# Kernel tuning notes

Hardware: AMD Instinct MI355X
Metric: run time of the kernel (lower is better)

Reference implementation:

```python
import jax, jax.numpy as jnp
import numpy as np

EPS_LOG = 1e-10
DECAY = 0.99
RESET_THRESHOLD = 2


def setup_inputs() -> dict:
    key = jax.random.key(0)
    ks = jax.random.split(key, 8)
    B, C_in, T = 4, 1024, 2048
    K, D = 8192, 256
    N = B * T
    return {
        "z": jax.random.normal(ks[0], (B, C_in, T), dtype=jnp.float32),
        "u": jax.random.uniform(ks[1], (N, K), dtype=jnp.float32),
        "Wi": jax.random.normal(ks[2], (D, C_in), dtype=jnp.float32) * 0.02,
        "bi": jax.random.normal(ks[3], (D,), dtype=jnp.float32) * 0.02,
        "Wo": jax.random.normal(ks[4], (C_in, D), dtype=jnp.float32) * 0.02,
        "bo": jax.random.normal(ks[5], (C_in,), dtype=jnp.float32) * 0.02,
        "embedding": jax.random.normal(ks[6], (K, D), dtype=jnp.float32),
        "cluster_size": jnp.zeros((K,), dtype=jnp.float32),
    }


def reference(z, u, Wi, bi, Wo, bo, embedding, cluster_size):
    B, _, T = z.shape
    K, D = embedding.shape
    N = B * T

    # inproj: Conv1d with kernel_size=1 == pointwise linear over channel dim
    z_e = jnp.einsum('bit,di->bdt', z, Wi) + bi[None, :, None]  # (B, D, T)
    z_d = z_e.transpose(0, 2, 1).reshape(N, D)                   # (b t) d

    # squared-euclidean distances via norm expansion
    dist = ((z_d ** 2).sum(axis=1, keepdims=True)
            - 2.0 * (z_d @ embedding.T)
            + (embedding ** 2).sum(axis=1))                      # (N, K)

    # gumbel noise (training=True), softmax_temp = 1.0
    gumbel = -jnp.log(-jnp.log(u + EPS_LOG) + EPS_LOG)
    logits = -dist + gumbel
    y_soft = jax.nn.softmax(logits, axis=-1)                     # (N, K)

    z_q_flat = y_soft @ embedding                                # (N, D)

    # kl_div(log(avg+eps), uniform target of shape (N,K), reduction='sum')
    avg_probs = y_soft.mean(axis=0)                              # (K,)
    inv_k = 1.0 / K
    kl_loss = N * jnp.sum(inv_k * (jnp.log(inv_k) - jnp.log(avg_probs + EPS_LOG)))

    indices = jnp.argmax(y_soft, axis=1)                         # (N,) int

    z_q = z_q_flat.reshape(B, T, D).transpose(0, 2, 1)           # (B, D, T)
    vq_loss = jnp.mean((z_e - jax.lax.stop_gradient(z_q)) ** 2)

    # outproj: Conv1d kernel_size=1
    out = jnp.einsum('bdt,od->bot', z_q, Wo) + bo[None, :, None]  # (B, C_in, T)

    # box_result: active_num uses cluster_size BEFORE the EMA update
    active_num = (cluster_size > RESET_THRESHOLD).sum().astype(z.dtype)
    counts = jnp.zeros((K,), z.dtype).at[indices].add(1.0)       # one-hot column sums
    probs = counts / N                                           # == mean(one_hot, axis=0)
    perplexity = jnp.exp(-jnp.sum(probs * jnp.log(probs + EPS_LOG)))
    new_cluster_size = cluster_size * DECAY + counts * (1.0 - DECAY)

    return out, vq_loss, kl_loss, perplexity, active_num, new_cluster_size
```

## Files before the change

kernel.cpp:

```cpp
#include <hip/hip_runtime.h>
#include <hip/hip_fp16.h>


#define NROWS 8192
#define KCL   8192
#define DDIM  256
#define CIN   1024
#define TSEQ  2048
#define EPSL  1e-10f
#define MHAT  (-140.0f)

#define OUT_SC   (4*CIN*TSEQ)

#define ZD_OFF   0
#define ZQ_OFF   (NROWS*DDIM)
#define E2_OFF   (2*NROWS*DDIM)
#define CS_OFF   (E2_OFF + KCL)
#define CNT_OFF  (CS_OFF + KCL)
#define VQ_OFF   (CNT_OFF + KCL)
#define LINV_OFF (VQ_OFF + 4)

#define ZD2W   0
#define ZQ2W   2097152
#define EBW    4194304
#define ETW    5242880
#define WOBW   6291456
#define ZFW    6422528
#define E2W    7471104
#define C2W    7479296
#define LINVW  7487488
#define CSUMW  7495680
#define CNTW   7503872
#define VQW    7512064
#define PW     7512128
#define ENDW   (PW + 33554432)

using short8v = __attribute__((ext_vector_type(8))) short;
using short4v = __attribute__((ext_vector_type(4))) short;
using f32x16  = __attribute__((ext_vector_type(16))) float;

__device__ __forceinline__ ushort f2bf(float f) {
  unsigned int x = __float_as_uint(f);
  return (ushort)((x + 0x7FFFu + ((x >> 16) & 1u)) >> 16);
}
__device__ __forceinline__ float bf2f(ushort h) {
  return __uint_as_float(((unsigned int)h) << 16);
}
__device__ __forceinline__ short8v pack8(float4 a, float4 b) {
  short8v v;
  v[0] = (short)f2bf(a.x); v[1] = (short)f2bf(a.y);
  v[2] = (short)f2bf(a.z); v[3] = (short)f2bf(a.w);
  v[4] = (short)f2bf(b.x); v[5] = (short)f2bf(b.y);
  v[6] = (short)f2bf(b.z); v[7] = (short)f2bf(b.w);
  return v;
}
__device__ __forceinline__ void gload16(const void* g, void* l) {
  __builtin_amdgcn_global_load_lds(
      (const __attribute__((address_space(1))) unsigned int*)g,
      (__attribute__((address_space(3))) unsigned int*)l, 16, 0, 0);
}


__global__ __launch_bounds__(256) void e2_kernel(const float* __restrict__ E,
                                                 float* __restrict__ e2) {
  const int tid = threadIdx.x;
  const int k = blockIdx.x * 64 + (tid >> 2);
  const int p = tid & 3;
  const float* row = E + (size_t)k * DDIM + p * 64;
  float s = 0.f;
#pragma unroll
  for (int j = 0; j < 16; ++j) {
    const float4 v = *reinterpret_cast<const float4*>(row + j * 4);
    s += v.x * v.x + v.y * v.y + v.z * v.z + v.w * v.w;
  }
  s += __shfl_xor(s, 1);
  s += __shfl_xor(s, 2);
  if (p == 0) e2[k] = s;
}

__global__ __launch_bounds__(256) void e2c2_kernel(const float* __restrict__ E,
                                                   float* __restrict__ e2,
                                                   float* __restrict__ c2) {
  const int tid = threadIdx.x;
  const int k = blockIdx.x * 64 + (tid >> 2);
  const int p = tid & 3;
  const float* row = E + (size_t)k * DDIM + p * 64;
  float s = 0.f;
#pragma unroll
  for (int j = 0; j < 16; ++j) {
    const float4 v = *reinterpret_cast<const float4*>(row + j * 4);
    s += v.x * v.x + v.y * v.y + v.z * v.z + v.w * v.w;
  }
  s += __shfl_xor(s, 1);
  s += __shfl_xor(s, 2);
  if (p == 0) { e2[k] = s; c2[k] = -s - MHAT; }
}

__global__ __launch_bounds__(256) void cvtwob_kernel(const float* __restrict__ W,
                                                     ushort* __restrict__ Wb) {
  const size_t i = ((size_t)blockIdx.x * 256 + threadIdx.x) * 8;
  const float4 a = *reinterpret_cast<const float4*>(W + i);
  const float4 b = *reinterpret_cast<const float4*>(W + i + 4);
  *reinterpret_cast<short8v*>(Wb + i) = pack8(a, b);
}

__global__ __launch_bounds__(256) void etprep_kernel(const float* __restrict__ E,
                                                     ushort* __restrict__ ET,
                                                     ushort* __restrict__ EB) {
  __shared__ float tb[64 * 68];
  const int t = threadIdx.x;
  const int kb = (blockIdx.x & 127) * 64;
  const int db = (blockIdx.x >> 7) * 64;
#pragma unroll
  for (int it = 0; it < 4; ++it) {
    const int r = (t >> 4) + it * 16;
    const int c = (t & 15) * 4;
    const float4 v = *reinterpret_cast<const float4*>(E + (size_t)(kb + r) * DDIM + db + c);
    tb[r * 68 + c] = v.x; tb[r * 68 + c + 1] = v.y;
    tb[r * 68 + c + 2] = v.z; tb[r * 68 + c + 3] = v.w;
    short4v o;
    o[0] = (short)f2bf(v.x); o[1] = (short)f2bf(v.y);
    o[2] = (short)f2bf(v.z); o[3] = (short)f2bf(v.w);
    *reinterpret_cast<short4v*>(EB + (size_t)(kb + r) * DDIM + db + c) = o;
  }
  __syncthreads();
  const int dl = t >> 2, kg = (t & 3) * 16;
  short8v o0, o1;
#pragma unroll
  for (int j = 0; j < 8; ++j) o0[j] = (short)f2bf(tb[(kg + j) * 68 + dl]);
#pragma unroll
  for (int j = 0; j < 8; ++j) o1[j] = (short)f2bf(tb[(kg + 8 + j) * 68 + dl]);
  ushort* dst = ET + (size_t)(db + dl) * KCL + kb + kg;
  *reinterpret_cast<short8v*>(dst) = o0;
  *reinterpret_cast<short8v*>(dst + 8) = o1;
}

__global__ __launch_bounds__(256) void cvtzf_kernel(const float* __restrict__ zd,
                                                    ushort* __restrict__ zf) {
  const int t = threadIdx.x;
  const int g = blockIdx.x;
  const int lane = t & 63, row = lane & 31, half = lane >> 5;
  const float* zr = zd + (size_t)(g * 32 + row) * DDIM + half * 8;
  ushort* dst = zf + ((size_t)g * 16 * 64 + lane) * 8;
#pragma unroll
  for (int i = 0; i < 4; ++i) {
    const int ks = (t >> 6) * 4 + i;
    const float4 a = *reinterpret_cast<const float4*>(zr + ks * 16);
    const float4 b = *reinterpret_cast<const float4*>(zr + ks * 16 + 4);
    *reinterpret_cast<short8v*>(dst + (size_t)ks * 64 * 8) = pack8(a, b);
  }
}

__global__ __launch_bounds__(256) void inproj_kernel(const float* __restrict__ z,
                                                     const float* __restrict__ Wi,
                                                     const float* __restrict__ bi,
                                                     float* __restrict__ zd) {
  __shared__ float wi_s[32 * 260];
  __shared__ float zc[32 * 64];
  const int tid = threadIdx.x;
  const int n0 = blockIdx.x * 64;
  const int b = n0 / TSEQ;
  const int t0 = n0 % TSEQ;
  const float* zb = z + (size_t)b * CIN * TSEQ;

  const int dg = tid & 63;
  const int d0 = dg * 4;
  const int wv = tid >> 6;
  const int r0 = wv * 16;

  float acc[4][16];
#pragma unroll
  for (int c = 0; c < 4; ++c)
#pragma unroll
    for (int r = 0; r < 16; ++r) acc[c][r] = 0.f;

  for (int i0 = 0; i0 < CIN; i0 += 32) {
    __syncthreads();
    {
      const int iiq = (tid & 7) * 4;
      const int dt = tid >> 3;
#pragma unroll
      for (int p = 0; p < 8; ++p) {
        const int d = dt + p * 32;
        const float4 w = *reinterpret_cast<const float4*>(Wi + (size_t)d * CIN + i0 + iiq);
        wi_s[(iiq + 0) * 260 + d] = w.x;
        wi_s[(iiq + 1) * 260 + d] = w.y;
        wi_s[(iiq + 2) * 260 + d] = w.z;
        wi_s[(iiq + 3) * 260 + d] = w.w;
      }
      const int rr = tid & 63;
      const int iib = tid >> 6;
#pragma unroll
      for (int p = 0; p < 8; ++p) {
        const int ii = iib + p * 4;
        zc[ii * 64 + rr] = zb[(size_t)(i0 + ii) * TSEQ + t0 + rr];
      }
    }
    __syncthreads();
#pragma unroll
    for (int ii = 0; ii < 32; ++ii) {
      const float4 w = *reinterpret_cast<const float4*>(&wi_s[ii * 260 + d0]);
#pragma unroll
      for (int rq = 0; rq < 4; ++rq) {
        const float4 zv = *reinterpret_cast<const float4*>(&zc[ii * 64 + r0 + rq * 4]);
        const float zz[4] = {zv.x, zv.y, zv.z, zv.w};
#pragma unroll
        for (int q = 0; q < 4; ++q) {
          acc[0][rq * 4 + q] += w.x * zz[q];
          acc[1][rq * 4 + q] += w.y * zz[q];
          acc[2][rq * 4 + q] += w.z * zz[q];
          acc[3][rq * 4 + q] += w.w * zz[q];
        }
      }
    }
  }
  const float4 bv = *reinterpret_cast<const float4*>(bi + d0);
#pragma unroll
  for (int r = 0; r < 16; ++r) {
    float4 o;
    o.x = acc[0][r] + bv.x;
    o.y = acc[1][r] + bv.y;
    o.z = acc[2][r] + bv.z;
    o.w = acc[3][r] + bv.w;
    *reinterpret_cast<float4*>(zd + (size_t)(n0 + r0 + r) * DDIM + d0) = o;
  }
}

#define FSTEP(KT, CUR, UC, UN)                                                 \
  {                                                                            \
    const int k0 = kbase + (KT) * 32;                                          \
    __syncthreads();            \
    if ((KT) < 15) {                                                           \
      _Pragma("unroll")                                                        \
      for (int pp = 0; pp < 2; ++pp) {                                         \
        const int q = tid + pp * 512, r = q >> 5, c = q & 31;                  \
        gload16(Eb + (size_t)(k0 + 32 + r) * 256 + (size_t)(c ^ (r & 7)) * 8,  \
                &Es[(1 - (CUR)) * 8192 + q * 8]);                              \
      }                                                                        \
      const float* ubn = ubase + k0 + 32 + r31;                                \
      _Pragma("unroll")                                                        \
      for (int reg = 0; reg < 16; ++reg) {                                     \
        const int dr = (reg & 3) + 8 * (reg >> 2);                             \
        UN[reg] = ubn[(size_t)dr << 13];                                       \
      }                                                                        \
    }                                                                          \
    const float ce = c2[k0 + r31];                                             \
    const ushort* Ecur = Es + (CUR) * 8192;                                    \
    f32x16 acc;                                                                \
    _Pragma("unroll")                                                          \
    for (int i = 0; i < 16; ++i) acc[i] = 0.f;                                 \
    _Pragma("unroll")                                                          \
    for (int ks = 0; ks < 16; ++ks) {                                          \
      const int cc = (ks * 2 + half) ^ (r31 & 7);                              \
      const short8v B =                                                        \
          *reinterpret_cast<const short8v*>(Ecur + r31 * 256 + cc * 8);        \
      acc = __builtin_amdgcn_mfma_f32_32x32x16_bf16(A[ks], B, acc, 0, 0, 0);   \
    }                                                                          \
    ushort* pdst = P + (size_t)rowu * KCL + k0 + r31;                          \
    _Pragma("unroll")                                                          \
    for (int reg = 0; reg < 16; ++reg) {                                       \
      const int dr = (reg & 3) + 8 * (reg >> 2);                               \
      const float D = 1e-10f - __logf(UC[reg] + 1e-10f);                       \
      const float pe = __fdividef(__expf(fmaf(acc[reg], 2.f, ce)), D);         \
      pdst[(size_t)dr << 13] = f2bf(pe);                                       \
    }                                                                          \
  }

__global__ __launch_bounds__(512, 2) void flash4_kernel(
    const ushort* __restrict__ ZF, const float* __restrict__ u,
    const ushort* __restrict__ Eb, const float* __restrict__ c2,
    ushort* __restrict__ P) {
  __shared__ ushort Es[2 * 32 * 256];
  const int tid = threadIdx.x;
  const int l = tid & 63, w = tid >> 6;
  const int half = l >> 5;
  const int nb = blockIdx.x & 31, kq = blockIdx.x >> 5;
  const int n0 = nb * 256;
  const int kbase = kq * 512;
  const int r31 = l & 31;

  short8v A[16];
  {
    const ushort* zf = ZF + ((size_t)(nb * 8 + w) * 16 * 64 + l) * 8;
#pragma unroll
    for (int ks = 0; ks < 16; ++ks)
      A[ks] = *reinterpret_cast<const short8v*>(zf + (size_t)ks * 512);
  }

  const int rowu = n0 + w * 32 + 4 * half;
  const float* ubase = u + ((size_t)rowu << 13);

#pragma unroll
  for (int pp = 0; pp < 2; ++pp) {
    const int q = tid + pp * 512, r = q >> 5, c = q & 31;
    gload16(Eb + (size_t)(kbase + r) * 256 + (size_t)(c ^ (r & 7)) * 8, &Es[q * 8]);
  }
  float uA[16], uB[16];
  {
    const float* ub = ubase + kbase + r31;
#pragma unroll
    for (int reg = 0; reg < 16; ++reg) {
      const int dr = (reg & 3) + 8 * (reg >> 2);
      uA[reg] = ub[(size_t)dr << 13];
    }
  }

  for (int kt2 = 0; kt2 < 16; kt2 += 2) {
    FSTEP(kt2, 0, uA, uB);
    FSTEP(kt2 + 1, 1, uB, uA);
  }
}

__global__ __launch_bounds__(256) void rowpass_kernel(
    const ushort* __restrict__ P, const float* __restrict__ zd,
    const float* __restrict__ E, const float* __restrict__ e2,
    const float* __restrict__ u, float* __restrict__ linv,
    float* __restrict__ counts) {
  const int l = threadIdx.x & 63;
  const int w = threadIdx.x >> 6;
  const int n = blockIdx.x * 4 + w;
  const ushort* pr = P + (size_t)n * KCL;
  float lsum = 0.f;
  float bv[4] = {-1.f, -1.f, -1.f, -1.f};
  int bi[4] = {0x7fffffff, 0x7fffffff, 0x7fffffff, 0x7fffffff};
  for (int it = 0; it < 16; ++it) {
    const short8v v = *reinterpret_cast<const short8v*>(pr + it * 512 + l * 8);
#pragma unroll
    for (int j = 0; j < 8; ++j) {
      const float f = bf2f((ushort)v[j]);
      lsum += f;
      const int kk = it * 512 + l * 8 + j;
      const bool c0 = f > bv[0], c1 = f > bv[1], c2 = f > bv[2], c3 = f > bv[3];
      const float n3 = c2 ? bv[2] : f; const int i3 = c2 ? bi[2] : kk;
      const float n2 = c1 ? bv[1] : f; const int i2 = c1 ? bi[1] : kk;
      const float n1 = c0 ? bv[0] : f; const int i1 = c0 ? bi[0] : kk;
      bv[3] = c3 ? n3 : bv[3]; bi[3] = c3 ? i3 : bi[3];
      bv[2] = c2 ? n2 : bv[2]; bi[2] = c2 ? i2 : bi[2];
      bv[1] = c1 ? n1 : bv[1]; bi[1] = c1 ? i1 : bi[1];
      bv[0] = c0 ? f : bv[0];  bi[0] = c0 ? kk : bi[0];
    }
  }
#pragma unroll
  for (int mk = 1; mk < 64; mk <<= 1) {
    lsum += __shfl_xor(lsum, mk);
    float ov[4]; int oi[4];
#pragma unroll
    for (int i = 0; i < 4; ++i) { ov[i] = __shfl_xor(bv[i], mk); oi[i] = __shfl_xor(bi[i], mk); }
#pragma unroll
    for (int i = 0; i < 4; ++i) {
      const float f = ov[i]; const int kk = oi[i];
      const bool c0 = (f > bv[0]) || (f == bv[0] && kk < bi[0]);
      const bool c1 = (f > bv[1]) || (f == bv[1] && kk < bi[1]);
      const bool c2 = (f > bv[2]) || (f == bv[2] && kk < bi[2]);
      const bool c3 = (f > bv[3]) || (f == bv[3] && kk < bi[3]);
      const float n3 = c2 ? bv[2] : f; const int i3 = c2 ? bi[2] : kk;
      const float n2 = c1 ? bv[1] : f; const int i2 = c1 ? bi[1] : kk;
      const float n1 = c0 ? bv[0] : f; const int i1 = c0 ? bi[0] : kk;
      bv[3] = c3 ? n3 : bv[3]; bi[3] = c3 ? i3 : bi[3];
      bv[2] = c2 ? n2 : bv[2]; bi[2] = c2 ? i2 : bi[2];
      bv[1] = c1 ? n1 : bv[1]; bi[1] = c1 ? i1 : bi[1];
      bv[0] = c0 ? f : bv[0];  bi[0] = c0 ? kk : bi[0];
    }
  }
  const float4 zv = *reinterpret_cast<const float4*>(zd + (size_t)n * DDIM + l * 4);
  float best = -1e30f; int besti = 0x7fffffff;
#pragma unroll
  for (int c = 0; c < 4; ++c) {
    const int kc = bi[c];
    const float4 ev = *reinterpret_cast<const float4*>(E + (size_t)kc * DDIM + l * 4);
    float d = zv.x * ev.x + zv.y * ev.y + zv.z * ev.z + zv.w * ev.w;
#pragma unroll
    for (int mk = 1; mk < 64; mk <<= 1) d += __shfl_xor(d, mk);
    const float uu = u[(size_t)n * KCL + kc];
    const float D = 1e-10f - __logf(uu + 1e-10f);
    const float g = -__logf(D);
    const float lg = 2.f * d - e2[kc] + g;
    if (lg > best || (lg == best && kc < besti)) { best = lg; besti = kc; }
  }
  if (l == 0) {
    atomicAdd(&counts[besti], 1.f);
    linv[n] = 1.f / lsum;
  }
}

__global__ __launch_bounds__(256) void colsum2_kernel(const ushort* __restrict__ P,
                                                      const float* __restrict__ linv,
                                                      float* __restrict__ colsum) {
  __shared__ float cs[512];
  const int t = threadIdx.x;
  cs[t] = 0.f; cs[t + 256] = 0.f;
  __syncthreads();
  const int kb = blockIdx.x & 15;
  const int nb = blockIdx.x >> 4;
  const int k0 = kb * 512 + (t & 63) * 8;
  const int r0 = nb * 256 + (t >> 6);
  float a[8] = {0.f, 0.f, 0.f, 0.f, 0.f, 0.f, 0.f, 0.f};
  for (int i = 0; i < 64; ++i) {
    const int n = r0 + i * 4;
    const float lv = linv[n];
    const short8v v = *reinterpret_cast<const short8v*>(P + (size_t)n * KCL + k0);
#pragma unroll
    for (int j = 0; j < 8; ++j) a[j] += bf2f((ushort)v[j]) * lv;
  }
#pragma unroll
  for (int j = 0; j < 8; ++j) atomicAdd(&cs[(t & 63) * 8 + j], a[j]);
  __syncthreads();
  atomicAdd(&colsum[kb * 512 + t], cs[t]);
  atomicAdd(&colsum[kb * 512 + t + 256], cs[t + 256]);
}

__global__ __launch_bounds__(512, 2) void pv2_kernel(
    const ushort* __restrict__ P, const ushort* __restrict__ ET,
    float* __restrict__ parts) {
  __shared__ ushort ps[64 * 64];
  __shared__ ushort es[256 * 64];
  const int tid = threadIdx.x;
  const int l = tid & 63, w = tid >> 6;
  const int half = l >> 5;
  const int r31 = l & 31;
  const int nb = blockIdx.x & 127, ks = blockIdx.x >> 7;
  const int n0 = nb * 64;
  const int kc0 = ks * 2048;
  const int nw = w & 1, dw = w >> 1;

  f32x16 acc0, acc1;
#pragma unroll
  for (int i = 0; i < 16; ++i) { acc0[i] = 0.f; acc1[i] = 0.f; }

  short8v rp, re[4];
  {
    const int r = tid >> 3, c = tid & 7;
    rp = *reinterpret_cast<const short8v*>(P + (size_t)(n0 + r) * KCL + kc0 + c * 8);
#pragma unroll
    for (int pp = 0; pp < 4; ++pp) {
      const int q = tid * 4 + pp; const int rr = q >> 3, cc = q & 7;
      re[pp] = *reinterpret_cast<const short8v*>(ET + (size_t)rr * KCL + kc0 + cc * 8);
    }
  }
  for (int t = 0; t < 32; ++t) {
    {
      const int r = tid >> 3, c = tid & 7;
      *reinterpret_cast<short8v*>(ps + r * 64 + ((c ^ (r & 7))) * 8) = rp;
    }
#pragma unroll
    for (int pp = 0; pp < 4; ++pp) {
      const int q = tid * 4 + pp; const int rr = q >> 3, cc = q & 7;
      *reinterpret_cast<short8v*>(es + rr * 64 + ((cc ^ (rr & 7))) * 8) = re[pp];
    }
    __syncthreads();
    if (t < 31) {
      const int kc = kc0 + (t + 1) * 64;
      {
        const int r = tid >> 3, c = tid & 7;
        rp = *reinterpret_cast<const short8v*>(P + (size_t)(n0 + r) * KCL + kc + c * 8);
      }
#pragma unroll
      for (int pp = 0; pp < 4; ++pp) {
        const int q = tid * 4 + pp; const int rr = q >> 3, cc = q & 7;
        re[pp] = *reinterpret_cast<const short8v*>(ET + (size_t)rr * KCL + kc + cc * 8);
      }
    }
#pragma unroll
    for (int ksn = 0; ksn < 4; ++ksn) {
      const int cc = ksn * 2 + half;
      short8v a, b0, b1;
      { const int r = nw * 32 + r31;      a  = *reinterpret_cast<const short8v*>(ps + r * 64 + ((cc ^ (r & 7))) * 8); }
      { const int r = dw * 64 + r31;      b0 = *reinterpret_cast<const short8v*>(es + r * 64 + ((cc ^ (r & 7))) * 8); }
      { const int r = dw * 64 + 32 + r31; b1 = *reinterpret_cast<const short8v*>(es + r * 64 + ((cc ^ (r & 7))) * 8); }
      acc0 = __builtin_amdgcn_mfma_f32_32x32x16_bf16(a, b0, acc0, 0, 0, 0);
      acc1 = __builtin_amdgcn_mfma_f32_32x32x16_bf16(a, b1, acc1, 0, 0, 0);
    }
    __syncthreads();
  }
  float* pbase = parts + (size_t)ks * NROWS * DDIM;
#pragma unroll
  for (int reg = 0; reg < 16; ++reg) {
    const int dr = (reg & 3) + 8 * (reg >> 2) + 4 * half;
    float* zr = pbase + (size_t)(n0 + nw * 32 + dr) * DDIM + dw * 64 + r31;
    zr[0]  = acc0[reg];
    zr[32] = acc1[reg];
  }
}

__global__ __launch_bounds__(256) void zqred_kernel(const float* __restrict__ parts,
                                                    const float* __restrict__ linv,
                                                    const float* __restrict__ zd,
                                                    float* __restrict__ zq,
                                                    float* __restrict__ vqs) {
  const size_t i = ((size_t)blockIdx.x * 256 + threadIdx.x) * 8;
  const int n = (int)(i >> 8);
  const float lv = linv[n];
  float s = 0.f;
#pragma unroll
  for (int j = 0; j < 8; j += 4) {
    float4 p0 = *reinterpret_cast<const float4*>(parts + i + j);
    const float4 p1 = *reinterpret_cast<const float4*>(parts + i + j + (size_t)NROWS * DDIM);
    const float4 p2 = *reinterpret_cast<const float4*>(parts + i + j + (size_t)2 * NROWS * DDIM);
    const float4 p3 = *reinterpret_cast<const float4*>(parts + i + j + (size_t)3 * NROWS * DDIM);
    const float4 a = *reinterpret_cast<const float4*>(zd + i + j);
    float4 o;
    o.x = (p0.x + p1.x + p2.x + p3.x) * lv;
    o.y = (p0.y + p1.y + p2.y + p3.y) * lv;
    o.z = (p0.z + p1.z + p2.z + p3.z) * lv;
    o.w = (p0.w + p1.w + p2.w + p3.w) * lv;
    *reinterpret_cast<float4*>(zq + i + j) = o;
    const float dx = a.x - o.x, dy = a.y - o.y, dz = a.z - o.z, dw = a.w - o.w;
    s += dx * dx + dy * dy + dz * dz + dw * dw;
  }
#pragma unroll
  for (int mk = 1; mk < 64; mk <<= 1) s += __shfl_xor(s, mk);
  if ((threadIdx.x & 63) == 0) atomicAdd(vqs, s);
}

__global__ __launch_bounds__(256) void outproj2_kernel(const float* __restrict__ zq,
                                                       const ushort* __restrict__ Wob,
                                                       const float* __restrict__ bo,
                                                       float* __restrict__ outp) {
  extern __shared__ char smem[];
  ushort* zs = (ushort*)smem;
  ushort* wsld = zs + 64 * 256;
  const int tid = threadIdx.x;
  const int l = tid & 63, w = tid >> 6;
  const int half = l >> 5;
  const int nb = blockIdx.x >> 4, ob = blockIdx.x & 15;
  const int n0 = nb * 64, o0 = ob * 64;
  const int nw = w & 1, ow = w >> 1;
  {
    const int row = tid >> 2, seg = tid & 3;
    const float* zr = zq + (size_t)(n0 + row) * DDIM + seg * 64;
    const ushort* wr = Wob + (size_t)(o0 + row) * DDIM + seg * 64;
#pragma unroll
    for (int g = 0; g < 8; ++g) {
      const float4 a = *reinterpret_cast<const float4*>(zr + g * 8);
      const float4 b = *reinterpret_cast<const float4*>(zr + g * 8 + 4);
      const int c = seg * 8 + g;
      *reinterpret_cast<short8v*>(zs + row * 256 + ((c ^ (row & 7))) * 8) = pack8(a, b);
      const short8v wv = *reinterpret_cast<const short8v*>(wr + g * 8);
      *reinterpret_cast<short8v*>(wsld + row * 256 + ((c ^ (row & 7))) * 8) = wv;
    }
  }
  __syncthreads();
  f32x16 acc;
#pragma unroll
  for (int i = 0; i < 16; ++i) acc[i] = 0.f;
#pragma unroll
  for (int ksn = 0; ksn < 16; ++ksn) {
    const int cc = ksn * 2 + half;
    const int ra = nw * 32 + (l & 31);
    const int rb = ow * 32 + (l & 31);
    const short8v a = *reinterpret_cast<const short8v*>(zs + ra * 256 + ((cc ^ (ra & 7))) * 8);
    const short8v b = *reinterpret_cast<const short8v*>(wsld + rb * 256 + ((cc ^ (rb & 7))) * 8);
    acc = __builtin_amdgcn_mfma_f32_32x32x16_bf16(a, b, acc, 0, 0, 0);
  }
  const int o = o0 + ow * 32 + (l & 31);
  const float bv = bo[o];
  const int nbase = n0 + nw * 32 + 4 * half;
#pragma unroll
  for (int rq = 0; rq < 4; ++rq) {
    const int n = nbase + rq * 8;
    const int b = n >> 11;
    const int tt = n & 2047;
    float4 ov;
    ov.x = acc[rq * 4 + 0] + bv;
    ov.y = acc[rq * 4 + 1] + bv;
    ov.z = acc[rq * 4 + 2] + bv;
    ov.w = acc[rq * 4 + 3] + bv;
    *reinterpret_cast<float4*>(outp + ((size_t)b * CIN + o) * TSEQ + tt) = ov;
  }
}

template <bool STORE_LG>
__global__ __launch_bounds__(512) void flash_kernel(
    const float* __restrict__ zd, const float* __restrict__ u,
    const float* __restrict__ E, const float* __restrict__ e2g,
    float* __restrict__ zq, float* __restrict__ colsum,
    float* __restrict__ counts, float* __restrict__ vqsum,
    float* __restrict__ linvg, __half* __restrict__ lgbuf) {
  extern __shared__ float lds[];
  float* zs = lds;
  float* es = zs + 32 * 260;
  float* e2t = es + 64 * 260;
  float* cst = e2t + 64;
  float* red = cst + 64;

  const int tid = threadIdx.x;
  const int lane = tid & 63;
  const int wv = tid >> 6;
  const int r = (lane >> 4) & 3;
  const int kg = lane & 15;
  const int row = wv * 4 + r;
  const int n0 = blockIdx.x * 32;
  const int n = n0 + row;

  {
    const int rr = tid >> 4;
    const int iq = tid & 15;
#pragma unroll
    for (int p = 0; p < 4; ++p) {
      const int i = iq * 16 + p * 4;
      *reinterpret_cast<float4*>(&zs[rr * 260 + i]) =
          *reinterpret_cast<const float4*>(zd + (size_t)(n0 + rr) * DDIM + i);
    }
  }

  float4 accp[4];
#pragma unroll
  for (int s = 0; s < 4; ++s) accp[s] = make_float4(0.f, 0.f, 0.f, 0.f);
  float lsum = 0.f;
  float best = -1e30f;
  int bidx = 0;

  const float* zrow = zs + row * 260;

  for (int t = 0; t < KCL / 64; ++t) {
    const int k0 = t * 64;
    __syncthreads();
    {
      const int iq = tid & 15;
#pragma unroll
      for (int pp = 0; pp < 2; ++pp) {
        const int kk = (tid >> 4) + pp * 32;
#pragma unroll
        for (int p = 0; p < 4; ++p) {
          const int i = iq * 16 + p * 4;
          *reinterpret_cast<float4*>(&es[kk * 260 + i]) =
              *reinterpret_cast<const float4*>(E + (size_t)(k0 + kk) * DDIM + i);
        }
      }
      if (tid < 64) e2t[tid] = e2g[k0 + tid];
    }
    __syncthreads();

    float acc4[4] = {0.f, 0.f, 0.f, 0.f};
#pragma unroll 4
    for (int i = 0; i < DDIM; i += 4) {
      const float4 zv = *reinterpret_cast<const float4*>(zrow + i);
#pragma unroll
      for (int jj = 0; jj < 4; ++jj) {
        const float4 ev = *reinterpret_cast<const float4*>(&es[(kg + jj * 16) * 260 + i]);
        acc4[jj] += zv.x * ev.x + zv.y * ev.y + zv.z * ev.z + zv.w * ev.w;
      }
    }

    float p4[4];
    float tmax = -1e30f;
    int tidx = 0;
#pragma unroll
    for (int jj = 0; jj < 4; ++jj) {
      const int kk = kg + jj * 16;
      const float uu = u[(size_t)n * KCL + k0 + kk];
      const float g = -__logf(-__logf(uu + EPSL) + EPSL);
      const float lt = 2.f * acc4[jj] - e2t[kk] + g - MHAT;
      const float pe = __expf(lt);
      p4[jj] = pe;
      lsum += pe;
      if (lt > tmax) { tmax = lt; tidx = k0 + kk; }
    }
#pragma unroll
    for (int mk = 1; mk <= 8; mk <<= 1) {
      const float ov = __shfl_xor(tmax, mk);
      const int oi = __shfl_xor(tidx, mk);
      if (ov > tmax || (ov == tmax && oi < tidx)) { tmax = ov; tidx = oi; }
    }
    if (tmax > best) { best = tmax; bidx = tidx; }

#pragma unroll
    for (int jj = 0; jj < 4; ++jj) {
#pragma unroll 4
      for (int q = 0; q < 16; ++q) {
        const int kk = jj * 16 + q;
        const float yv = __shfl(p4[jj], (lane & 48) | q);
        const float* erow = &es[kk * 260 + kg * 16];
#pragma unroll
        for (int s = 0; s < 4; ++s) {
          const int c = (s + kg) & 3;
          const float4 ev = *reinterpret_cast<const float4*>(erow + c * 4);
          accp[s].x += yv * ev.x;
          accp[s].y += yv * ev.y;
          accp[s].z += yv * ev.z;
          accp[s].w += yv * ev.w;
        }
      }
    }
  }

#pragma unroll
  for (int mk = 1; mk <= 8; mk <<= 1) lsum += __shfl_xor(lsum, mk);
  const float linv = 1.0f / lsum;

  if (kg == 0) {
    atomicAdd(&counts[bidx], 1.0f);
    linvg[n] = linv;
  }

  float vqp = 0.f;
#pragma unroll
  for (int s = 0; s < 4; ++s) {
    const int c = (s + kg) & 3;
    const int d = kg * 16 + c * 4;
    float4 o;
    o.x = accp[s].x * linv;
    o.y = accp[s].y * linv;
    o.z = accp[s].z * linv;
    o.w = accp[s].w * linv;
    *reinterpret_cast<float4*>(zq + (size_t)n * DDIM + d) = o;
    const float4 zv = *reinterpret_cast<const float4*>(zrow + d);
    const float dx = zv.x - o.x, dy = zv.y - o.y, dz = zv.z - o.z, dw = zv.w - o.w;
    vqp += dx * dx + dy * dy + dz * dz + dw * dw;
  }
#pragma unroll
  for (int mk = 1; mk <= 32; mk <<= 1) vqp += __shfl_xor(vqp, mk);
  if (lane == 0) red[wv] = vqp;
  __syncthreads();
  if (tid == 0) {
    float s = 0.f;
#pragma unroll
    for (int ww = 0; ww < 8; ++ww) s += red[ww];
    atomicAdd(vqsum, s);
  }

  if (!STORE_LG) {
    if (tid < 64) cst[tid] = 0.f;
    for (int t = 0; t < KCL / 64; ++t) {
      const int k0 = t * 64;
      __syncthreads();
      {
        const int iq = tid & 15;
#pragma unroll
        for (int pp = 0; pp < 2; ++pp) {
          const int kk = (tid >> 4) + pp * 32;
#pragma unroll
          for (int p = 0; p < 4; ++p) {
            const int i = iq * 16 + p * 4;
            *reinterpret_cast<float4*>(&es[kk * 260 + i]) =
                *reinterpret_cast<const float4*>(E + (size_t)(k0 + kk) * DDIM + i);
          }
        }
        if (tid < 64) e2t[tid] = e2g[k0 + tid];
      }
      __syncthreads();
      float acc4[4] = {0.f, 0.f, 0.f, 0.f};
#pragma unroll 4
      for (int i = 0; i < DDIM; i += 4) {
        const float4 zv = *reinterpret_cast<const float4*>(zrow + i);
#pragma unroll
        for (int jj = 0; jj < 4; ++jj) {
          const float4 ev = *reinterpret_cast<const float4*>(&es[(kg + jj * 16) * 260 + i]);
          acc4[jj] += zv.x * ev.x + zv.y * ev.y + zv.z * ev.z + zv.w * ev.w;
        }
      }
      float cs4[4];
#pragma unroll
      for (int jj = 0; jj < 4; ++jj) {
        const int kk = kg + jj * 16;
        const float uu = u[(size_t)n * KCL + k0 + kk];
        const float g = -__logf(-__logf(uu + EPSL) + EPSL);
        const float lt = 2.f * acc4[jj] - e2t[kk] + g - MHAT;
        cs4[jj] = __expf(lt) * linv;
      }
#pragma unroll
      for (int mk = 16; mk <= 32; mk <<= 1)
#pragma unroll
        for (int jj = 0; jj < 4; ++jj) cs4[jj] += __shfl_xor(cs4[jj], mk);
      if (lane < 16) {
#pragma unroll
        for (int jj = 0; jj < 4; ++jj) atomicAdd(&cst[kg + jj * 16], cs4[jj]);
      }
      __syncthreads();
      if (tid < 64) {
        atomicAdd(&colsum[k0 + tid], cst[tid]);
        cst[tid] = 0.f;
      }
    }
  }
}

__global__ __launch_bounds__(256) void outproj_kernel(const float* __restrict__ zq,
                                                      const float* __restrict__ Wo,
                                                      const float* __restrict__ bo,
                                                      float* __restrict__ outp) {
  __shared__ float wo_s[32 * 260];
  __shared__ float zc[32 * 68];
  const int tid = threadIdx.x;
  const int n0 = (blockIdx.x >> 2) * 64;
  const int ot = (blockIdx.x & 3) * 256;
  const int b = n0 / TSEQ;
  const int t0 = n0 % TSEQ;

  const int og = tid & 63;
  const int o0 = og * 4;
  const int wv = tid >> 6;
  const int r0 = wv * 16;

  float acc[4][16];
#pragma unroll
  for (int c = 0; c < 4; ++c)
#pragma unroll
    for (int r = 0; r < 16; ++r) acc[c][r] = 0.f;

  for (int dd = 0; dd < DDIM; dd += 32) {
    __syncthreads();
    {
      const int ccq = (tid & 7) * 4;
      const int oq = tid >> 3;
#pragma unroll
      for (int p = 0; p < 8; ++p) {
        const int oo = oq + p * 32;
        const float4 w = *reinterpret_cast<const float4*>(Wo + (size_t)(ot + oo) * DDIM + dd + ccq);
        wo_s[(ccq + 0) * 260 + oo] = w.x;
        wo_s[(ccq + 1) * 260 + oo] = w.y;
        wo_s[(ccq + 2) * 260 + oo] = w.z;
        wo_s[(ccq + 3) * 260 + oo] = w.w;
      }
#pragma unroll
      for (int p = 0; p < 2; ++p) {
        const int rr = oq + p * 32;
        const float4 v = *reinterpret_cast<const float4*>(zq + (size_t)(n0 + rr) * DDIM + dd + ccq);
        zc[(ccq + 0) * 68 + rr] = v.x;
        zc[(ccq + 1) * 68 + rr] = v.y;
        zc[(ccq + 2) * 68 + rr] = v.z;
        zc[(ccq + 3) * 68 + rr] = v.w;
      }
    }
    __syncthreads();
#pragma unroll
    for (int cc = 0; cc < 32; ++cc) {
      const float4 w = *reinterpret_cast<const float4*>(&wo_s[cc * 260 + o0]);
#pragma unroll
      for (int rq = 0; rq < 4; ++rq) {
        const float4 zv = *reinterpret_cast<const float4*>(&zc[cc * 68 + r0 + rq * 4]);
        const float zz[4] = {zv.x, zv.y, zv.z, zv.w};
#pragma unroll
        for (int q = 0; q < 4; ++q) {
          acc[0][rq * 4 + q] += w.x * zz[q];
          acc[1][rq * 4 + q] += w.y * zz[q];
          acc[2][rq * 4 + q] += w.z * zz[q];
          acc[3][rq * 4 + q] += w.w * zz[q];
        }
      }
    }
  }
  const float4 bv = *reinterpret_cast<const float4*>(bo + ot + o0);
  float* ob = outp + (size_t)b * CIN * TSEQ + t0;
  const float bb[4] = {bv.x, bv.y, bv.z, bv.w};
#pragma unroll
  for (int c = 0; c < 4; ++c) {
#pragma unroll
    for (int rq = 0; rq < 4; ++rq) {
      float4 o;
      o.x = acc[c][rq * 4 + 0] + bb[c];
      o.y = acc[c][rq * 4 + 1] + bb[c];
      o.z = acc[c][rq * 4 + 2] + bb[c];
      o.w = acc[c][rq * 4 + 3] + bb[c];
      *reinterpret_cast<float4*>(ob + (size_t)(ot + o0 + c) * TSEQ + r0 + rq * 4) = o;
    }
  }
}

__global__ __launch_bounds__(256) void finalize_kernel(
    const float* __restrict__ colsum, const float* __restrict__ counts,
    const float* __restrict__ vqsum, const float* __restrict__ csin,
    float* __restrict__ outsc, float* __restrict__ ncs) {
  __shared__ float rS[3][4];
  const int tid = threadIdx.x;
  const int lane = tid & 63;
  const int wv = tid >> 6;
  float sLog = 0.f, sH = 0.f, sAct = 0.f;
  for (int k = tid; k < KCL; k += 256) {
    const float avg = colsum[k] * (1.0f / NROWS);
    sLog += __logf(avg + EPSL);
    const float pb = counts[k] * (1.0f / NROWS);
    sH += pb * __logf(pb + EPSL);
    sAct += (csin[k] > 2.0f) ? 1.f : 0.f;
    ncs[k] = csin[k] * 0.99f + counts[k] * 0.01f;
  }
#pragma unroll
  for (int mk = 1; mk <= 32; mk <<= 1) {
    sLog += __shfl_xor(sLog, mk);
    sH += __shfl_xor(sH, mk);
    sAct += __shfl_xor(sAct, mk);
  }
  if (lane == 0) { rS[0][wv] = sLog; rS[1][wv] = sH; rS[2][wv] = sAct; }
  __syncthreads();
  if (tid == 0) {
    float SL = 0.f, SH = 0.f, SA = 0.f;
#pragma unroll
    for (int w = 0; w < 4; ++w) { SL += rS[0][w]; SH += rS[1][w]; SA += rS[2][w]; }
    outsc[0] = vqsum[0] * (1.0f / ((float)NROWS * (float)DDIM));
    outsc[1] = (float)NROWS * __logf(1.0f / (float)KCL) - SL;
    outsc[2] = __expf(-SH);
    outsc[3] = SA;
  }
}

extern "C" void kernel_launch(void* const* d_in, const int* in_sizes, int n_in,
                              void* d_out, int out_size, void* d_ws, size_t ws_size,
                              hipStream_t stream) {
  (void)in_sizes; (void)n_in; (void)out_size;
  const float* z = (const float*)d_in[0];
  const float* u = (const float*)d_in[1];
  const float* Wi = (const float*)d_in[2];
  const float* bi = (const float*)d_in[3];
  const float* Wo = (const float*)d_in[4];
  const float* bo = (const float*)d_in[5];
  const float* E = (const float*)d_in[6];
  const float* csin = (const float*)d_in[7];
  float* outp = (float*)d_out;
  float* ws = (float*)d_ws;

  const size_t needNew = (size_t)ENDW * 4;
  if (ws_size >= needNew) {
    ushort* EB = (ushort*)(ws + EBW);
    ushort* ET = (ushort*)(ws + ETW);
    ushort* WOB = (ushort*)(ws + WOBW);
    ushort* ZF = (ushort*)(ws + ZFW);
    ushort* P = (ushort*)(ws + PW);

    hipMemsetAsync((void*)(ws + CSUMW), 0, (size_t)(2 * KCL + 64) * 4, stream);

    e2c2_kernel<<<KCL / 64, 256, 0, stream>>>(E, ws + E2W, ws + C2W);
    etprep_kernel<<<512, 256, 0, stream>>>(E, ET, EB);
    cvtwob_kernel<<<128, 256, 0, stream>>>(Wo, WOB);
    inproj_kernel<<<NROWS / 64, 256, 0, stream>>>(z, Wi, bi, ws + ZD2W);
    cvtzf_kernel<<<NROWS / 32, 256, 0, stream>>>(ws + ZD2W, ZF);

    flash4_kernel<<<512, 512, 0, stream>>>(ZF, u, EB, ws + C2W, P);
    rowpass_kernel<<<NROWS / 4, 256, 0, stream>>>(P, ws + ZD2W, E, ws + E2W, u,
                                                  ws + LINVW, ws + CNTW);
    colsum2_kernel<<<512, 256, 0, stream>>>(P, ws + LINVW, ws + CSUMW);
    pv2_kernel<<<512, 512, 0, stream>>>(P, ET, outp);
    zqred_kernel<<<1024, 256, 0, stream>>>(outp, ws + LINVW, ws + ZD2W,
                                           ws + ZQ2W, ws + VQW);

    hipFuncSetAttribute(reinterpret_cast<const void*>(&outproj2_kernel),
                        hipFuncAttributeMaxDynamicSharedMemorySize, 65536);
    outproj2_kernel<<<2048, 256, 65536, stream>>>(ws + ZQ2W, WOB, bo, outp);
    finalize_kernel<<<1, 256, 0, stream>>>(ws + CSUMW, ws + CNTW, ws + VQW,
                                           csin, outp + OUT_SC, outp + OUT_SC + 4);
  } else {
    hipMemsetAsync((void*)(ws + CS_OFF), 0, (size_t)(2 * KCL + 1) * sizeof(float), stream);
    e2_kernel<<<KCL / 64, 256, 0, stream>>>(E, ws + E2_OFF);
    inproj_kernel<<<NROWS / 64, 256, 0, stream>>>(z, Wi, bi, ws + ZD_OFF);
    const int ldsB = (32 * 260 + 64 * 260 + 64 + 64 + 16) * 4;
    hipFuncSetAttribute(reinterpret_cast<const void*>(&flash_kernel<false>),
                        hipFuncAttributeMaxDynamicSharedMemorySize, ldsB);
    flash_kernel<false><<<NROWS / 32, 512, ldsB, stream>>>(
        ws + ZD_OFF, u, E, ws + E2_OFF, ws + ZQ_OFF, ws + CS_OFF, ws + CNT_OFF,
        ws + VQ_OFF, ws + LINV_OFF, (__half*)nullptr);
    outproj_kernel<<<(NROWS / 64) * 4, 256, 0, stream>>>(ws + ZQ_OFF, Wo, bo, outp);
    finalize_kernel<<<1, 256, 0, stream>>>(ws + CS_OFF, ws + CNT_OFF, ws + VQ_OFF,
                                           csin, outp + OUT_SC, outp + OUT_SC + 4);
  }
}
```

Before: 542.6 us.

## Split inproj over channels, shrink flash blocks, fuse rowpass with column sums

The input projection now splits the 1024-channel reduction across two blocks and combines the halves into a zeroed buffer with atomicAdd. This gives 512 blocks instead of 128 so more of the GPU is busy. The flash kernel moves from 512-thread blocks over 256 rows to 128-thread blocks over 64 rows (2048 blocks, 3 per CU) for better occupancy and load balance. The row pass (softmax sum and top-4 argmax) is fused with the column-sum pass so each 32-row tile of P is reread while still hot in cache, which removes one kernel launch. In exchange it adds many float atomics on zd and colsum, an extra memset, and a less coalesced row-scan access pattern.

Result: slower. 718.8 us (+32.5%).

```diff
diff --git a/kernel.cpp b/kernel.cpp
--- a/kernel.cpp
+++ b/kernel.cpp
@@ -151,30 +151,32 @@
   }
 }
 
-__global__ __launch_bounds__(256) void inproj_kernel(const float* __restrict__ z,
-                                                     const float* __restrict__ Wi,
-                                                     const float* __restrict__ bi,
-                                                     float* __restrict__ zd) {
+__global__ __launch_bounds__(256) void inproj32_kernel(const float* __restrict__ z,
+                                                       const float* __restrict__ Wi,
+                                                       const float* __restrict__ bi,
+                                                       float* __restrict__ zd) {
   __shared__ float wi_s[32 * 260];
-  __shared__ float zc[32 * 64];
+  __shared__ float zc[32 * 32];
   const int tid = threadIdx.x;
-  const int n0 = blockIdx.x * 64;
+  const int nb = blockIdx.x >> 1, cih = blockIdx.x & 1;
+  const int n0 = nb * 32;
   const int b = n0 / TSEQ;
   const int t0 = n0 % TSEQ;
   const float* zb = z + (size_t)b * CIN * TSEQ;
+  const int ibase = cih * 512;
 
   const int dg = tid & 63;
   const int d0 = dg * 4;
   const int wv = tid >> 6;
-  const int r0 = wv * 16;
-
-  float acc[4][16];
+  const int r0 = wv * 8;
+
+  float acc[4][8];
 #pragma unroll
   for (int c = 0; c < 4; ++c)
 #pragma unroll
-    for (int r = 0; r < 16; ++r) acc[c][r] = 0.f;
-
-  for (int i0 = 0; i0 < CIN; i0 += 32) {
+    for (int r = 0; r < 8; ++r) acc[c][r] = 0.f;
+
+  for (int i0 = ibase; i0 < ibase + 512; i0 += 32) {
     __syncthreads();
     {
       const int iiq = (tid & 7) * 4;
@@ -188,12 +190,12 @@
         wi_s[(iiq + 2) * 260 + d] = w.z;
         wi_s[(iiq + 3) * 260 + d] = w.w;
       }
-      const int rr = tid & 63;
-      const int iib = tid >> 6;
-#pragma unroll
-      for (int p = 0; p < 8; ++p) {
-        const int ii = iib + p * 4;
-        zc[ii * 64 + rr] = zb[(size_t)(i0 + ii) * TSEQ + t0 + rr];
+      const int rr = tid & 31;
+      const int iib = tid >> 5;
+#pragma unroll
+      for (int p = 0; p < 4; ++p) {
+        const int ii = iib + p * 8;
+        zc[ii * 32 + rr] = zb[(size_t)(i0 + ii) * TSEQ + t0 + rr];
       }
     }
     __syncthreads();
@@ -201,8 +203,8 @@
     for (int ii = 0; ii < 32; ++ii) {
       const float4 w = *reinterpret_cast<const float4*>(&wi_s[ii * 260 + d0]);
 #pragma unroll
-      for (int rq = 0; rq < 4; ++rq) {
-        const float4 zv = *reinterpret_cast<const float4*>(&zc[ii * 64 + r0 + rq * 4]);
+      for (int rq = 0; rq < 2; ++rq) {
+        const float4 zv = *reinterpret_cast<const float4*>(&zc[ii * 32 + r0 + rq * 4]);
         const float zz[4] = {zv.x, zv.y, zv.z, zv.w};
 #pragma unroll
         for (int q = 0; q < 4; ++q) {
@@ -215,25 +217,26 @@
     }
   }
   const float4 bv = *reinterpret_cast<const float4*>(bi + d0);
-#pragma unroll
-  for (int r = 0; r < 16; ++r) {
-    float4 o;
-    o.x = acc[0][r] + bv.x;
-    o.y = acc[1][r] + bv.y;
-    o.z = acc[2][r] + bv.z;
-    o.w = acc[3][r] + bv.w;
-    *reinterpret_cast<float4*>(zd + (size_t)(n0 + r0 + r) * DDIM + d0) = o;
-  }
-}
-
-#define FSTEP(KT, CUR, UC, UN)                                                 \
+  const float bx = cih ? 0.f : bv.x, by = cih ? 0.f : bv.y;
+  const float bz = cih ? 0.f : bv.z, bw = cih ? 0.f : bv.w;
+#pragma unroll
+  for (int r = 0; r < 8; ++r) {
+    float* zr = zd + (size_t)(n0 + r0 + r) * DDIM + d0;
+    atomicAdd(zr + 0, acc[0][r] + bx);
+    atomicAdd(zr + 1, acc[1][r] + by);
+    atomicAdd(zr + 2, acc[2][r] + bz);
+    atomicAdd(zr + 3, acc[3][r] + bw);
+  }
+}
+
+#define FSTEP5(KT, CUR, UC, UN)                                                \
   {                                                                            \
     const int k0 = kbase + (KT) * 32;                                          \
-    __syncthreads();            \
+    __syncthreads();              \
     if ((KT) < 15) {                                                           \
       _Pragma("unroll")                                                        \
-      for (int pp = 0; pp < 2; ++pp) {                                         \
-        const int q = tid + pp * 512, r = q >> 5, c = q & 31;                  \
+      for (int pp = 0; pp < 8; ++pp) {                                         \
+        const int q = tid + pp * 128, r = q >> 5, c = q & 31;                  \
         gload16(Eb + (size_t)(k0 + 32 + r) * 256 + (size_t)(c ^ (r & 7)) * 8,  \
                 &Es[(1 - (CUR)) * 8192 + q * 8]);                              \
       }                                                                        \
@@ -266,7 +269,7 @@
     }                                                                          \
   }
 
-__global__ __launch_bounds__(512, 2) void flash4_kernel(
+__global__ __launch_bounds__(128, 3) void flash5_kernel(
     const ushort* __restrict__ ZF, const float* __restrict__ u,
     const ushort* __restrict__ Eb, const float* __restrict__ c2,
     ushort* __restrict__ P) {
@@ -274,14 +277,14 @@
   const int tid = threadIdx.x;
   const int l = tid & 63, w = tid >> 6;
   const int half = l >> 5;
-  const int nb = blockIdx.x & 31, kq = blockIdx.x >> 5;
-  const int n0 = nb * 256;
+  const int nb = blockIdx.x & 127, kq = blockIdx.x >> 7;
+  const int n0 = nb * 64;
   const int kbase = kq * 512;
   const int r31 = l & 31;
 
   short8v A[16];
   {
-    const ushort* zf = ZF + ((size_t)(nb * 8 + w) * 16 * 64 + l) * 8;
+    const ushort* zf = ZF + ((size_t)(nb * 2 + w) * 16 * 64 + l) * 8;
 #pragma unroll
     for (int ks = 0; ks < 16; ++ks)
       A[ks] = *reinterpret_cast<const short8v*>(zf + (size_t)ks * 512);
@@ -291,8 +294,8 @@
   const float* ubase = u + ((size_t)rowu << 13);
 
 #pragma unroll
-  for (int pp = 0; pp < 2; ++pp) {
-    const int q = tid + pp * 512, r = q >> 5, c = q & 31;
+  for (int pp = 0; pp < 8; ++pp) {
+    const int q = tid + pp * 128, r = q >> 5, c = q & 31;
     gload16(Eb + (size_t)(kbase + r) * 256 + (size_t)(c ^ (r & 7)) * 8, &Es[q * 8]);
   }
   float uA[16], uB[16];
@@ -306,30 +309,33 @@
   }
 
   for (int kt2 = 0; kt2 < 16; kt2 += 2) {
-    FSTEP(kt2, 0, uA, uB);
-    FSTEP(kt2 + 1, 1, uB, uA);
-  }
-}
-
-__global__ __launch_bounds__(256) void rowpass_kernel(
+    FSTEP5(kt2, 0, uA, uB);
+    FSTEP5(kt2 + 1, 1, uB, uA);
+  }
+}
+
+__global__ __launch_bounds__(256) void rcpass_kernel(
     const ushort* __restrict__ P, const float* __restrict__ zd,
     const float* __restrict__ E, const float* __restrict__ e2,
-    const float* __restrict__ u, float* __restrict__ linv,
-    float* __restrict__ counts) {
-  const int l = threadIdx.x & 63;
-  const int w = threadIdx.x >> 6;
-  const int n = blockIdx.x * 4 + w;
-  const ushort* pr = P + (size_t)n * KCL;
+    const float* __restrict__ u, float* __restrict__ linvg,
+    float* __restrict__ counts, float* __restrict__ colsum) {
+  __shared__ float linv_s[32];
+  const int t = threadIdx.x;
+  const int n0 = blockIdx.x * 32;
+  const int row = t >> 3, seg = t & 7;
+  const int n = n0 + row;
+
+  const ushort* pr = P + (size_t)n * KCL + seg * 8;
   float lsum = 0.f;
   float bv[4] = {-1.f, -1.f, -1.f, -1.f};
   int bi[4] = {0x7fffffff, 0x7fffffff, 0x7fffffff, 0x7fffffff};
-  for (int it = 0; it < 16; ++it) {
-    const short8v v = *reinterpret_cast<const short8v*>(pr + it * 512 + l * 8);
+  for (int it = 0; it < 128; ++it) {
+    const short8v v = *reinterpret_cast<const short8v*>(pr + it * 64);
 #pragma unroll
     for (int j = 0; j < 8; ++j) {
       const float f = bf2f((ushort)v[j]);
       lsum += f;
-      const int kk = it * 512 + l * 8 + j;
+      const int kk = seg * 8 + it * 64 + j;
       const bool c0 = f > bv[0], c1 = f > bv[1], c2 = f > bv[2], c3 = f > bv[3];
       const float n3 = c2 ? bv[2] : f; const int i3 = c2 ? bi[2] : kk;
       const float n2 = c1 ? bv[1] : f; const int i2 = c1 ? bi[1] : kk;
@@ -341,7 +347,7 @@
     }
   }
 #pragma unroll
-  for (int mk = 1; mk < 64; mk <<= 1) {
+  for (int mk = 1; mk <= 4; mk <<= 1) {
     lsum += __shfl_xor(lsum, mk);
     float ov[4]; int oi[4];
 #pragma unroll
@@ -362,51 +368,53 @@
       bv[0] = c0 ? f : bv[0];  bi[0] = c0 ? kk : bi[0];
     }
   }
-  const float4 zv = *reinterpret_cast<const float4*>(zd + (size_t)n * DDIM + l * 4);
+  float4 zq4[8];
+#pragma unroll
+  for (int q = 0; q < 8; ++q)
+    zq4[q] = *reinterpret_cast<const float4*>(zd + (size_t)n * DDIM + seg * 32 + q * 4);
   float best = -1e30f; int besti = 0x7fffffff;
 #pragma unroll
   for (int c = 0; c < 4; ++c) {
     const int kc = bi[c];
-    const float4 ev = *reinterpret_cast<const float4*>(E + (size_t)kc * DDIM + l * 4);
-    float d = zv.x * ev.x + zv.y * ev.y + zv.z * ev.z + zv.w * ev.w;
-#pragma unroll
-    for (int mk = 1; mk < 64; mk <<= 1) d += __shfl_xor(d, mk);
+    const float* er = E + (size_t)kc * DDIM + seg * 32;
+    float d = 0.f;
+#pragma unroll
+    for (int q = 0; q < 8; ++q) {
+      const float4 ev = *reinterpret_cast<const float4*>(er + q * 4);
+      d += zq4[q].x * ev.x + zq4[q].y * ev.y + zq4[q].z * ev.z + zq4[q].w * ev.w;
+    }
+#pragma unroll
+    for (int mk = 1; mk <= 4; mk <<= 1) d += __shfl_xor(d, mk);
     const float uu = u[(size_t)n * KCL + kc];
     const float D = 1e-10f - __logf(uu + 1e-10f);
     const float g = -__logf(D);
     const float lg = 2.f * d - e2[kc] + g;
     if (lg > best || (lg == best && kc < besti)) { best = lg; besti = kc; }
   }
-  if (l == 0) {
+  if (seg == 0) {
     atomicAdd(&counts[besti], 1.f);
-    linv[n] = 1.f / lsum;
-  }
-}
-
-__global__ __launch_bounds__(256) void colsum2_kernel(const ushort* __restrict__ P,
-                                                      const float* __restrict__ linv,
-                                                      float* __restrict__ colsum) {
-  __shared__ float cs[512];
-  const int t = threadIdx.x;
-  cs[t] = 0.f; cs[t + 256] = 0.f;
+    const float li = 1.f / lsum;
+    linvg[n] = li;
+    linv_s[row] = li;
+  }
   __syncthreads();
-  const int kb = blockIdx.x & 15;
-  const int nb = blockIdx.x >> 4;
-  const int k0 = kb * 512 + (t & 63) * 8;
-  const int r0 = nb * 256 + (t >> 6);
-  float a[8] = {0.f, 0.f, 0.f, 0.f, 0.f, 0.f, 0.f, 0.f};
-  for (int i = 0; i < 64; ++i) {
-    const int n = r0 + i * 4;
-    const float lv = linv[n];
-    const short8v v = *reinterpret_cast<const short8v*>(P + (size_t)n * KCL + k0);
-#pragma unroll
-    for (int j = 0; j < 8; ++j) a[j] += bf2f((ushort)v[j]) * lv;
-  }
-#pragma unroll
-  for (int j = 0; j < 8; ++j) atomicAdd(&cs[(t & 63) * 8 + j], a[j]);
-  __syncthreads();
-  atomicAdd(&colsum[kb * 512 + t], cs[t]);
-  atomicAdd(&colsum[kb * 512 + t + 256], cs[t + 256]);
+
+  float acc2[32];
+#pragma unroll
+  for (int j = 0; j < 32; ++j) acc2[j] = 0.f;
+  const ushort* pc = P + (size_t)n0 * KCL + t * 32;
+  for (int r = 0; r < 32; ++r) {
+    const float lv = linv_s[r];
+    const ushort* prr = pc + (size_t)r * KCL;
+#pragma unroll
+    for (int g4 = 0; g4 < 4; ++g4) {
+      const short8v v = *reinterpret_cast<const short8v*>(prr + g4 * 8);
+#pragma unroll
+      for (int j = 0; j < 8; ++j) acc2[g4 * 8 + j] += bf2f((ushort)v[j]) * lv;
+    }
+  }
+#pragma unroll
+  for (int j = 0; j < 32; ++j) atomicAdd(&colsum[t * 32 + j], acc2[j]);
 }
 
 __global__ __launch_bounds__(512, 2) void pv2_kernel(
@@ -553,7 +561,7 @@
     acc = __builtin_amdgcn_mfma_f32_32x32x16_bf16(a, b, acc, 0, 0, 0);
   }
   const int o = o0 + ow * 32 + (l & 31);
-  const float bv = bo[o];
+  const float bvv = bo[o];
   const int nbase = n0 + nw * 32 + 4 * half;
 #pragma unroll
   for (int rq = 0; rq < 4; ++rq) {
@@ -561,10 +569,10 @@
     const int b = n >> 11;
     const int tt = n & 2047;
     float4 ov;
-    ov.x = acc[rq * 4 + 0] + bv;
-    ov.y = acc[rq * 4 + 1] + bv;
-    ov.z = acc[rq * 4 + 2] + bv;
-    ov.w = acc[rq * 4 + 3] + bv;
+    ov.x = acc[rq * 4 + 0] + bvv;
+    ov.y = acc[rq * 4 + 1] + bvv;
+    ov.z = acc[rq * 4 + 2] + bvv;
+    ov.w = acc[rq * 4 + 3] + bvv;
     *reinterpret_cast<float4*>(outp + ((size_t)b * CIN + o) * TSEQ + tt) = ov;
   }
 }
@@ -917,17 +925,17 @@
     ushort* P = (ushort*)(ws + PW);
 
     hipMemsetAsync((void*)(ws + CSUMW), 0, (size_t)(2 * KCL + 64) * 4, stream);
+    hipMemsetAsync((void*)(ws + ZD2W), 0, (size_t)NROWS * DDIM * 4, stream);
 
     e2c2_kernel<<<KCL / 64, 256, 0, stream>>>(E, ws + E2W, ws + C2W);
     etprep_kernel<<<512, 256, 0, stream>>>(E, ET, EB);
     cvtwob_kernel<<<128, 256, 0, stream>>>(Wo, WOB);
-    inproj_kernel<<<NROWS / 64, 256, 0, stream>>>(z, Wi, bi, ws + ZD2W);
+    inproj32_kernel<<<512, 256, 0, stream>>>(z, Wi, bi, ws + ZD2W);
     cvtzf_kernel<<<NROWS / 32, 256, 0, stream>>>(ws + ZD2W, ZF);
 
-    flash4_kernel<<<512, 512, 0, stream>>>(ZF, u, EB, ws + C2W, P);
-    rowpass_kernel<<<NROWS / 4, 256, 0, stream>>>(P, ws + ZD2W, E, ws + E2W, u,
-                                                  ws + LINVW, ws + CNTW);
-    colsum2_kernel<<<512, 256, 0, stream>>>(P, ws + LINVW, ws + CSUMW);
+    flash5_kernel<<<2048, 128, 0, stream>>>(ZF, u, EB, ws + C2W, P);
+    rcpass_kernel<<<NROWS / 32, 256, 0, stream>>>(P, ws + ZD2W, E, ws + E2W, u,
+                                                  ws + LINVW, ws + CNTW, ws + CSUMW);
     pv2_kernel<<<512, 512, 0, stream>>>(P, ET, outp);
     zqred_kernel<<<1024, 256, 0, stream>>>(outp, ws + LINVW, ws + ZD2W,
                                            ws + ZQ2W, ws + VQW);
@@ -939,8 +947,9 @@
                                            csin, outp + OUT_SC, outp + OUT_SC + 4);
   } else {
     hipMemsetAsync((void*)(ws + CS_OFF), 0, (size_t)(2 * KCL + 1) * sizeof(float), stream);
+    hipMemsetAsync((void*)(ws + ZD_OFF), 0, (size_t)NROWS * DDIM * 4, stream);
     e2_kernel<<<KCL / 64, 256, 0, stream>>>(E, ws + E2_OFF);
-    inproj_kernel<<<NROWS / 64, 256, 0, stream>>>(z, Wi, bi, ws + ZD_OFF);
+    inproj32_kernel<<<512, 256, 0, stream>>>(z, Wi, bi, ws + ZD_OFF);
     const int ldsB = (32 * 260 + 64 * 260 + 64 + 64 + 16) * 4;
     hipFuncSetAttribute(reinterpret_cast<const void*>(&flash_kernel<false>),
                         hipFuncAttributeMaxDynamicSharedMemorySize, ldsB);
```
